# Kernel tuning notes

Hardware: AMD Instinct MI355X
Metric: run time of the kernel (lower is better)

Reference implementation:

```python
import jax, jax.numpy as jnp
import numpy as np

B, N, D, H, T = 32, 4096, 256, 8, 28  # batch, nodes, hidden_dim, bottleneck_dim, horizon


def setup_inputs() -> dict:
    key = jax.random.key(0)
    ks = jax.random.split(key, 16)
    s = 0.1
    return {
        "x": jax.random.normal(ks[0], (B, N, D), jnp.float32),
        "last_step": jax.random.normal(ks[1], (B, N), jnp.float32),
        # GRU params (PyTorch layout: gates ordered r, z, n)
        "W_ih": jax.random.normal(ks[2], (3 * H, 1), jnp.float32) * s,
        "W_hh": jax.random.normal(ks[3], (3 * H, H), jnp.float32) * s,
        "b_ih": jax.random.normal(ks[4], (3 * H,), jnp.float32) * s,
        "b_hh": jax.random.normal(ks[5], (3 * H,), jnp.float32) * s,
        # hidden_proj: Linear(D -> H)
        "Wp": jax.random.normal(ks[6], (H, D), jnp.float32) * s,
        "bp": jax.random.normal(ks[7], (H,), jnp.float32) * s,
        # output_proj: Linear(H -> 1)
        "Wo": jax.random.normal(ks[8], (1, H), jnp.float32) * s,
        "bo": jax.random.normal(ks[9], (1,), jnp.float32) * s,
        # refine_gate: Linear(D->H), ReLU, Linear(H->T), Sigmoid
        "Wg1": jax.random.normal(ks[10], (H, D), jnp.float32) * s,
        "bg1": jax.random.normal(ks[11], (H,), jnp.float32) * s,
        "Wg2": jax.random.normal(ks[12], (T, H), jnp.float32) * s,
        "bg2": jax.random.normal(ks[13], (T,), jnp.float32) * s,
        "log_decay": jnp.float32(-2.3),
    }


def _rollout(x, last_step, W_ih, W_hh, b_ih, b_hh, Wp, bp, Wo, bo, Wg1, bg1, Wg2, bg2, log_decay):
    b, n, d = x.shape
    h = x.reshape(b * n, d) @ Wp.T + bp                 # [BN, H] initial GRU hidden
    cur = last_step.reshape(b * n)                       # scalar input per row
    w_ih = W_ih[:, 0]                                    # [3H] (input_size == 1)

    def step(carry, _):
        h, cur = carry
        gi = cur[:, None] * w_ih[None, :] + b_ih         # [BN, 3H]
        gh = h @ W_hh.T + b_hh                           # [BN, 3H]
        r = jax.nn.sigmoid(gi[:, :H] + gh[:, :H])
        z = jax.nn.sigmoid(gi[:, H:2 * H] + gh[:, H:2 * H])
        ncand = jnp.tanh(gi[:, 2 * H:] + r * gh[:, 2 * H:])
        h_new = (1.0 - z) * ncand + z * h
        pred = h_new @ Wo[0] + bo[0]                     # [BN]
        return (h_new, pred), pred

    (_, _), preds = jax.lax.scan(step, (h, cur), None, length=T)  # [T, BN]
    gru_pred = preds.T.reshape(b, n, T)                  # [B, N, T]

    gate = jax.nn.sigmoid(
        jax.nn.relu(jnp.einsum('bnd,hd->bnh', x, Wg1) + bg1) @ Wg2.T + bg2
    )                                                    # [B, N, T]
    time_steps = jnp.arange(1, T + 1, dtype=x.dtype)
    decay_curve = jnp.exp(-jnp.exp(log_decay) * time_steps)       # [T]
    decay_pred = last_step[..., None] * decay_curve               # [B, N, T]
    return gate * gru_pred + (1.0 - gate) * decay_pred


def reference(x, last_step, W_ih, W_hh, b_ih, b_hh, Wp, bp, Wo, bo, Wg1, bg1, Wg2, bg2, log_decay):
    return _rollout(x, last_step, W_ih, W_hh, b_ih, b_hh, Wp, bp, Wo, bo, Wg1, bg1, Wg2, bg2, log_decay)
```

## Files before the change

kernel.cpp:

```cpp
#include <hip/hip_runtime.h>

#define TT 28

typedef __attribute__((ext_vector_type(8))) short bf16x8;
typedef __attribute__((ext_vector_type(4))) float f32x4;

__device__ __forceinline__ unsigned fbits(float f){ union{float f; unsigned u;} v; v.f=f; return v.u; }
__device__ __forceinline__ float bitsf(unsigned u){ union{unsigned u; float f;} v; v.u=u; return v.f; }
__device__ __forceinline__ short bf16rnd(float f){ return (short)((fbits(f)+0x8000u)>>16); }

__global__ __launch_bounds__(256) __attribute__((amdgpu_waves_per_eu(2, 2)))
void horizon_kernel(
    const float* __restrict__ x, const float* __restrict__ last_step,
    const float* __restrict__ W_ih, const float* __restrict__ W_hh,
    const float* __restrict__ b_ih, const float* __restrict__ b_hh,
    const float* __restrict__ Wp, const float* __restrict__ bp,
    const float* __restrict__ Wo, const float* __restrict__ bo,
    const float* __restrict__ Wg1, const float* __restrict__ bg1,
    const float* __restrict__ Wg2, const float* __restrict__ bg2,
    const float* __restrict__ log_decay, float* __restrict__ out)
{
    __shared__ __attribute__((aligned(16))) float s_whh[24*8];
    __shared__ __attribute__((aligned(16))) float s_gate[28][12];
    __shared__ __attribute__((aligned(16))) float s_wiabc[32];
    __shared__ __attribute__((aligned(16))) float s_wb4[32];
    __shared__ __attribute__((aligned(16))) float s_dyn[4][64*29];

    const int tid = threadIdx.x;

    if (tid < 192) s_whh[tid] = W_hh[tid];
    if (tid < 224) s_gate[tid>>3][tid&7] = Wg2[tid];
    if (tid < 28)  s_gate[tid][8] = bg2[tid];
    if (tid < 16){ s_wiabc[2*tid] = W_ih[tid]; s_wiabc[2*tid+1] = b_ih[tid] + b_hh[tid]; }
    if (tid < 8){
        s_wb4[4*tid+0] = W_ih[16+tid];
        s_wb4[4*tid+1] = b_ih[16+tid];
        s_wb4[4*tid+2] = b_hh[16+tid];
        s_wb4[4*tid+3] = Wo[tid];
    }
    __syncthreads();

    const int lane = tid & 63;
    const int wv   = tid >> 6;
    const int c    = lane >> 4;
    const int rl   = lane & 15;
    const int group = blockIdx.x*4 + wv;
    float* dyn = &s_dyn[wv][0];

    const float* wrow = (rl < 8) ? (Wp + rl*256) : (Wg1 + (rl-8)*256);
    bf16x8 bfrag[8];
    #pragma unroll
    for (int kk=0; kk<8; ++kk){
        #pragma unroll
        for (int j=0; j<8; ++j) bfrag[kk][j] = bf16rnd(wrow[kk*32 + c*8 + j]);
    }
    const float aBias = (rl < 8) ? bp[rl] : bg1[rl-8];

    #pragma unroll 1
    for (int sub=0; sub<4; ++sub){
        const float* xrow = x + (size_t)(group*64 + sub*16 + rl) * 256;
        f32x4 acc = {0.f, 0.f, 0.f, 0.f};
        #pragma unroll
        for (int kk=0; kk<8; ++kk){
            float4 v0 = *(const float4*)(xrow + kk*32 + c*8);
            float4 v1 = *(const float4*)(xrow + kk*32 + c*8 + 4);
            float xs[8] = {v0.x,v0.y,v0.z,v0.w, v1.x,v1.y,v1.z,v1.w};
            bf16x8 ahi, alo;
            #pragma unroll
            for (int j=0; j<8; ++j){
                unsigned u  = fbits(xs[j]);
                unsigned hb = (u + 0x8000u) & 0xFFFF0000u;
                ahi[j] = (short)(hb >> 16);
                alo[j] = bf16rnd(xs[j] - bitsf(hb));
            }
            acc = __builtin_amdgcn_mfma_f32_16x16x32_bf16(ahi, bfrag[kk], acc, 0, 0, 0);
            acc = __builtin_amdgcn_mfma_f32_16x16x32_bf16(alo, bfrag[kk], acc, 0, 0, 0);
        }
        #pragma unroll
        for (int r=0; r<4; ++r){
            float v = acc[r] + aBias;
            if (rl >= 8) v = fmaxf(v, 0.f);
            dyn[(sub*16 + c*4 + r)*20 + rl] = v;
        }
    }

    float h[8], q[8];
    #pragma unroll
    for (int j=0; j<8; ++j){ h[j] = dyn[lane*20 + j]; q[j] = dyn[lane*20 + 8 + j]; }

    float w1[16], bb1[16];
    #pragma unroll
    for (int p=0; p<8; ++p){
        float4 wb = *(const float4*)&s_wiabc[p*4];
        w1[2*p] = wb.x; bb1[2*p] = wb.y; w1[2*p+1] = wb.z; bb1[2*p+1] = wb.w;
    }
    float w2[8], bi2[8], bh2c[8], wo8[8];
    #pragma unroll
    for (int j=0; j<8; ++j){
        float4 wb = *(const float4*)&s_wb4[4*j];
        w2[j] = wb.x; bi2[j] = wb.y; bh2c[j] = wb.z; wo8[j] = wb.w;
    }
    float whn[8][8];
    #pragma unroll
    for (int o=0; o<8; ++o){
        float4 wa = *(const float4*)&s_whh[(16+o)*8];
        float4 wc = *(const float4*)&s_whh[(16+o)*8+4];
        whn[o][0]=wa.x; whn[o][1]=wa.y; whn[o][2]=wa.z; whn[o][3]=wa.w;
        whn[o][4]=wc.x; whn[o][5]=wc.y; whn[o][6]=wc.z; whn[o][7]=wc.w;
    }

    const int lrow  = group*64 + lane;
    const float ls0 = last_step[lrow];
    float cur   = ls0;
    const float df = __expf(-__expf(log_decay[0]));
    float decay = 1.f;
    const float boS = bo[0];

    #pragma unroll 1
    for (int t=0; t<TT; ++t){
        asm volatile("" ::: "memory");

        float s[16];
        #pragma unroll
        for (int o=0; o<16; ++o) s[o] = fmaf(cur, w1[o], bb1[o]);
        #pragma unroll
        for (int o=0; o<16; ++o){
            float4 wa = *(const float4*)&s_whh[o*8];
            float4 wc = *(const float4*)&s_whh[o*8+4];
            float a = s[o];
            a = fmaf(wa.x,h[0],a); a = fmaf(wa.y,h[1],a); a = fmaf(wa.z,h[2],a); a = fmaf(wa.w,h[3],a);
            a = fmaf(wc.x,h[4],a); a = fmaf(wc.y,h[5],a); a = fmaf(wc.z,h[6],a); a = fmaf(wc.w,h[7],a);
            s[o] = a;
        }
        float nn[8], zz[8];
        #pragma unroll
        for (int o=0; o<8; ++o){
            float g = bh2c[o];
            g = fmaf(whn[o][0],h[0],g); g = fmaf(whn[o][1],h[1],g);
            g = fmaf(whn[o][2],h[2],g); g = fmaf(whn[o][3],h[3],g);
            g = fmaf(whn[o][4],h[4],g); g = fmaf(whn[o][5],h[5],g);
            g = fmaf(whn[o][6],h[6],g); g = fmaf(whn[o][7],h[7],g);
            float r  = 1.f/(1.f + __expf(-s[o]));
            float un = fmaf(r, g, fmaf(cur, w2[o], bi2[o]));
            float e2 = __expf(2.f*un);
            nn[o] = 1.f - 2.f/(e2 + 1.f);
            zz[o] = 1.f/(1.f + __expf(-s[8+o]));
        }
        float pred = boS;
        #pragma unroll
        for (int j=0; j<8; ++j){
            h[j] = fmaf(zz[j], h[j]-nn[j], nn[j]);
            pred = fmaf(h[j], wo8[j], pred);
        }
        float4 ga = *(const float4*)&s_gate[t][0];
        float4 gb = *(const float4*)&s_gate[t][4];
        float gl = s_gate[t][8];
        gl = fmaf(ga.x,q[0],gl); gl = fmaf(ga.y,q[1],gl); gl = fmaf(ga.z,q[2],gl); gl = fmaf(ga.w,q[3],gl);
        gl = fmaf(gb.x,q[4],gl); gl = fmaf(gb.y,q[5],gl); gl = fmaf(gb.z,q[6],gl); gl = fmaf(gb.w,q[7],gl);
        float gate = 1.f/(1.f + __expf(-gl));

        decay *= df;
        float dp = ls0 * decay;
        dyn[lane*29 + t] = fmaf(gate, pred - dp, dp);
        cur = pred;
    }

    float o28[TT];
    #pragma unroll
    for (int t=0; t<TT; ++t) o28[t] = dyn[lane*29 + t];
    float* orow = out + (size_t)lrow * TT;
    #pragma unroll
    for (int i=0; i<7; ++i){
        float4 v = make_float4(o28[4*i], o28[4*i+1], o28[4*i+2], o28[4*i+3]);
        *(float4*)(orow + 4*i) = v;
    }
}

extern "C" void kernel_launch(void* const* d_in, const int* in_sizes, int n_in,
                              void* d_out, int out_size, void* d_ws, size_t ws_size,
                              hipStream_t stream)
{
    const float* x         = (const float*)d_in[0];
    const float* last_step = (const float*)d_in[1];
    const float* W_ih      = (const float*)d_in[2];
    const float* W_hh      = (const float*)d_in[3];
    const float* b_ih      = (const float*)d_in[4];
    const float* b_hh      = (const float*)d_in[5];
    const float* Wp        = (const float*)d_in[6];
    const float* bp        = (const float*)d_in[7];
    const float* Wo        = (const float*)d_in[8];
    const float* bo        = (const float*)d_in[9];
    const float* Wg1       = (const float*)d_in[10];
    const float* bg1       = (const float*)d_in[11];
    const float* Wg2       = (const float*)d_in[12];
    const float* bg2       = (const float*)d_in[13];
    const float* log_decay = (const float*)d_in[14];

    hipLaunchKernelGGL(horizon_kernel, dim3(512), dim3(256), 0, stream,
                       x, last_step, W_ih, W_hh, b_ih, b_hh, Wp, bp, Wo, bo,
                       Wg1, bg1, Wg2, bg2, log_decay, (float*)d_out);
}
```

Baseline: 279.5 us.

## Use fp16 dot2 for GRU recurrence and fold log2e into weights

The GRU hidden-to-hidden matvec now uses packed fp16 dot2 instructions, with all 24x8 W_hh weights kept in registers as half pairs instead of being reloaded from shared memory every step. The log2(e) factors are pre-folded into the weights and biases so the sigmoid and tanh can use raw exp2 and reciprocal intrinsics. This cuts VALU and LDS work per timestep in the serial recurrence. The trade is fp16 rounding of the hidden state and weights across 28 steps, which may reduce accuracy, plus higher register pressure; the projection loop is also unrolled by two.

After: 258.5 us. -7.5%, faster.

```diff
diff --git a/kernel.cpp b/kernel.cpp
--- a/kernel.cpp
+++ b/kernel.cpp
@@ -1,13 +1,39 @@
 #include <hip/hip_runtime.h>
 
 #define TT 28
+#define L2E 1.4426950408889634f
 
 typedef __attribute__((ext_vector_type(8))) short bf16x8;
 typedef __attribute__((ext_vector_type(4))) float f32x4;
+typedef _Float16 h2 __attribute__((ext_vector_type(2)));
+typedef __fp16 fp16x2 __attribute__((ext_vector_type(2)));
 
 __device__ __forceinline__ unsigned fbits(float f){ union{float f; unsigned u;} v; v.f=f; return v.u; }
 __device__ __forceinline__ float bitsf(unsigned u){ union{unsigned u; float f;} v; v.u=u; return v.f; }
 __device__ __forceinline__ short bf16rnd(float f){ return (short)((fbits(f)+0x8000u)>>16); }
+
+__device__ __forceinline__ h2 PKH2(float a, float b){
+    fp16x2 t = __builtin_amdgcn_cvt_pkrtz(a, b);
+    return __builtin_bit_cast(h2, t);
+}
+
+#if __has_builtin(__builtin_amdgcn_fdot2)
+#define FDOT2(a,b,c) __builtin_amdgcn_fdot2((a),(b),(c),false)
+#else
+__device__ __forceinline__ float FDOT2(h2 a, h2 b, float c){
+    return fmaf((float)a.x,(float)b.x, fmaf((float)a.y,(float)b.y,(c)));
+}
+#endif
+#if __has_builtin(__builtin_amdgcn_exp2f)
+#define EXP2(x) __builtin_amdgcn_exp2f(x)
+#else
+#define EXP2(x) exp2f(x)
+#endif
+#if __has_builtin(__builtin_amdgcn_rcpf)
+#define RCP(x) __builtin_amdgcn_rcpf(x)
+#else
+#define RCP(x) (1.f/(x))
+#endif
 
 __global__ __launch_bounds__(256) __attribute__((amdgpu_waves_per_eu(2, 2)))
 void horizon_kernel(
@@ -28,14 +54,14 @@
 
     const int tid = threadIdx.x;
 
-    if (tid < 192) s_whh[tid] = W_hh[tid];
-    if (tid < 224) s_gate[tid>>3][tid&7] = Wg2[tid];
-    if (tid < 28)  s_gate[tid][8] = bg2[tid];
-    if (tid < 16){ s_wiabc[2*tid] = W_ih[tid]; s_wiabc[2*tid+1] = b_ih[tid] + b_hh[tid]; }
+    if (tid < 192) s_whh[tid] = W_hh[tid] * (tid < 128 ? L2E : 2.0f*L2E);
+    if (tid < 224) s_gate[tid>>3][tid&7] = Wg2[tid] * L2E;
+    if (tid < 28)  s_gate[tid][8] = bg2[tid] * L2E;
+    if (tid < 16){ s_wiabc[2*tid] = W_ih[tid]*L2E; s_wiabc[2*tid+1] = (b_ih[tid] + b_hh[tid])*L2E; }
     if (tid < 8){
-        s_wb4[4*tid+0] = W_ih[16+tid];
-        s_wb4[4*tid+1] = b_ih[16+tid];
-        s_wb4[4*tid+2] = b_hh[16+tid];
+        s_wb4[4*tid+0] = W_ih[16+tid]*2.0f*L2E;
+        s_wb4[4*tid+1] = b_ih[16+tid]*2.0f*L2E;
+        s_wb4[4*tid+2] = b_hh[16+tid]*2.0f*L2E;
         s_wb4[4*tid+3] = Wo[tid];
     }
     __syncthreads();
@@ -56,7 +82,7 @@
     }
     const float aBias = (rl < 8) ? bp[rl] : bg1[rl-8];
 
-    #pragma unroll 1
+    #pragma unroll 2
     for (int sub=0; sub<4; ++sub){
         const float* xrow = x + (size_t)(group*64 + sub*16 + rl) * 256;
         f32x4 acc = {0.f, 0.f, 0.f, 0.f};
@@ -100,13 +126,13 @@
         float4 wb = *(const float4*)&s_wb4[4*j];
         w2[j] = wb.x; bi2[j] = wb.y; bh2c[j] = wb.z; wo8[j] = wb.w;
     }
-    float whn[8][8];
-    #pragma unroll
-    for (int o=0; o<8; ++o){
-        float4 wa = *(const float4*)&s_whh[(16+o)*8];
-        float4 wc = *(const float4*)&s_whh[(16+o)*8+4];
-        whn[o][0]=wa.x; whn[o][1]=wa.y; whn[o][2]=wa.z; whn[o][3]=wa.w;
-        whn[o][4]=wc.x; whn[o][5]=wc.y; whn[o][6]=wc.z; whn[o][7]=wc.w;
+    h2 whh2[24][4];
+    #pragma unroll
+    for (int o=0; o<24; ++o){
+        float4 wa = *(const float4*)&s_whh[o*8];
+        float4 wc = *(const float4*)&s_whh[o*8+4];
+        whh2[o][0] = PKH2(wa.x, wa.y); whh2[o][1] = PKH2(wa.z, wa.w);
+        whh2[o][2] = PKH2(wc.x, wc.y); whh2[o][3] = PKH2(wc.z, wc.w);
     }
 
     const int lrow  = group*64 + lane;
@@ -118,33 +144,29 @@
 
     #pragma unroll 1
     for (int t=0; t<TT; ++t){
-        asm volatile("" ::: "memory");
+        h2 hh[4];
+        #pragma unroll
+        for (int k=0; k<4; ++k) hh[k] = PKH2(h[2*k], h[2*k+1]);
 
         float s[16];
         #pragma unroll
-        for (int o=0; o<16; ++o) s[o] = fmaf(cur, w1[o], bb1[o]);
-        #pragma unroll
         for (int o=0; o<16; ++o){
-            float4 wa = *(const float4*)&s_whh[o*8];
-            float4 wc = *(const float4*)&s_whh[o*8+4];
-            float a = s[o];
-            a = fmaf(wa.x,h[0],a); a = fmaf(wa.y,h[1],a); a = fmaf(wa.z,h[2],a); a = fmaf(wa.w,h[3],a);
-            a = fmaf(wc.x,h[4],a); a = fmaf(wc.y,h[5],a); a = fmaf(wc.z,h[6],a); a = fmaf(wc.w,h[7],a);
+            float a = fmaf(cur, w1[o], bb1[o]);
+            #pragma unroll
+            for (int k=0; k<4; ++k) a = FDOT2(hh[k], whh2[o][k], a);
             s[o] = a;
         }
         float nn[8], zz[8];
         #pragma unroll
         for (int o=0; o<8; ++o){
             float g = bh2c[o];
-            g = fmaf(whn[o][0],h[0],g); g = fmaf(whn[o][1],h[1],g);
-            g = fmaf(whn[o][2],h[2],g); g = fmaf(whn[o][3],h[3],g);
-            g = fmaf(whn[o][4],h[4],g); g = fmaf(whn[o][5],h[5],g);
-            g = fmaf(whn[o][6],h[6],g); g = fmaf(whn[o][7],h[7],g);
-            float r  = 1.f/(1.f + __expf(-s[o]));
+            #pragma unroll
+            for (int k=0; k<4; ++k) g = FDOT2(hh[k], whh2[16+o][k], g);
+            float r  = RCP(1.f + EXP2(-s[o]));
             float un = fmaf(r, g, fmaf(cur, w2[o], bi2[o]));
-            float e2 = __expf(2.f*un);
-            nn[o] = 1.f - 2.f/(e2 + 1.f);
-            zz[o] = 1.f/(1.f + __expf(-s[8+o]));
+            float e2 = EXP2(un);
+            nn[o] = fmaf(-2.f, RCP(e2 + 1.f), 1.f);
+            zz[o] = RCP(1.f + EXP2(-s[8+o]));
         }
         float pred = boS;
         #pragma unroll
@@ -157,7 +179,7 @@
         float gl = s_gate[t][8];
         gl = fmaf(ga.x,q[0],gl); gl = fmaf(ga.y,q[1],gl); gl = fmaf(ga.z,q[2],gl); gl = fmaf(ga.w,q[3],gl);
         gl = fmaf(gb.x,q[4],gl); gl = fmaf(gb.y,q[5],gl); gl = fmaf(gb.z,q[6],gl); gl = fmaf(gb.w,q[7],gl);
-        float gate = 1.f/(1.f + __expf(-gl));
+        float gate = RCP(1.f + EXP2(-gl));
 
         decay *= df;
         float dp = ls0 * decay;
```
